# Performance work log

Hardware: AMD Instinct MI355X
Metric: run time of the kernel (lower is better)

Reference implementation:

```python
import jax, jax.numpy as jnp
import numpy as np

NUM_HEADS = 8
C_DIM = 512


def setup_inputs() -> dict:
    key = jax.random.key(0)
    ks = jax.random.split(key, 10)
    B, K, C, H, W = 8, 4, C_DIM, 16, 16
    M = NUM_HEADS
    s = 0.02
    return {
        "content": jax.random.normal(ks[0], (B, C, H, W), jnp.float32),
        "refs": jax.random.normal(ks[1], (B, K, C, H, W), jnp.float32),
        "qW": jax.random.normal(ks[2], (C, C * M), jnp.float32) * s,
        "qb": jax.random.normal(ks[3], (C * M,), jnp.float32) * s,
        "kW": jax.random.normal(ks[4], (C, C * M), jnp.float32) * s,
        "kb": jax.random.normal(ks[5], (C * M,), jnp.float32) * s,
        "vW": jax.random.normal(ks[6], (C, C * M), jnp.float32) * s,
        "vb": jax.random.normal(ks[7], (C * M,), jnp.float32) * s,
        "fcW": jax.random.normal(ks[8], (C * M, C), jnp.float32) * s,
        "fcb": jax.random.normal(ks[9], (C,), jnp.float32) * s,
    }


def reference(content, refs, qW, qb, kW, kb, vW, vb, fcW, fcb):
    B, C, H, W = content.shape
    K = refs.shape[1]
    M = qW.shape[1] // C
    HW = H * W
    KHW = K * HW

    # b c h w -> b (h w) c
    cs = content.reshape(B, C, HW).transpose(0, 2, 1)
    # b k c h w -> b (k h w) c
    rs = refs.transpose(0, 1, 3, 4, 2).reshape(B, KHW, C)

    # projections; output channel layout is (c m): head m takes strided features
    q = (cs @ qW + qb).reshape(B, HW, C, M)      # b q c m
    k = (rs @ kW + kb).reshape(B, KHW, C, M)     # b k c m
    v = (rs @ vW + vb).reshape(B, KHW, C, M)     # b k c m

    scale = jnp.asarray(float(C) ** (M / 2.0), content.dtype)  # faithful: C**(num_heads/2)
    scores = jnp.einsum('bqcm,bkcm->bmqk', q, k) / scale
    attn = jax.nn.softmax(scores, axis=-1)
    # output concat is head-major: (m c)
    out = jnp.einsum('bmqk,bkcm->bqmc', attn, v).reshape(B, HW, M * C)

    res = out @ fcW + fcb                         # b (h w) c
    res = res.transpose(0, 2, 1).reshape(B, C, H, W)
    return jnp.concatenate([res, content], axis=1)
```

## Files before the change

### kernel.cpp

```cpp
#include <hip/hip_runtime.h>

#define B_   8
#define K_   4
#define C_   512
#define M_   8
#define HW_  256
#define CM_  4096

__global__ void k_rbar(const float* __restrict__ refs, float* __restrict__ rbar) {
    const int bc = blockIdx.x;
    const int b  = bc >> 9;
    const int c  = bc & (C_ - 1);
    const int t  = threadIdx.x;
    const int k   = t >> 6;
    const int hw4 = t & 63;

    const float4* p = (const float4*)refs
                    + ((((size_t)b * K_ + k) * C_ + c) << 6) + hw4;
    const float4 v = *p;
    float s = (v.x + v.y) + (v.z + v.w);

#pragma unroll
    for (int off = 32; off > 0; off >>= 1)
        s += __shfl_down(s, off, 64);

    __shared__ float wsum[4];
    if ((t & 63) == 0) wsum[t >> 6] = s;
    __syncthreads();
    if (t == 0)
        rbar[bc] = (wsum[0] + wsum[1] + wsum[2] + wsum[3]) * (1.0f / (K_ * HW_));
}

__global__ void k_vbar(const float* __restrict__ rbar, const float* __restrict__ vW,
                       const float* __restrict__ vb, float* __restrict__ of) {
    const int blk   = blockIdx.x;
    const int b     = blk >> 4;
    const int chunk = blk & 15;
    const int t     = threadIdx.x;
    const int cm    = chunk * 256 + t;

    __shared__ float rb[C_];
    for (int i = t; i < C_; i += 256) rb[i] = rbar[b * C_ + i];
    __syncthreads();

    float acc = 0.f;
#pragma unroll 8
    for (int c = 0; c < C_; ++c)
        acc += rb[c] * vW[(size_t)c * CM_ + cm];

    const int ci = cm >> 3;
    const int m  = cm & 7;
    of[b * CM_ + m * C_ + ci] = acc + vb[cm];
}

__global__ void k_res(const float* __restrict__ of, const float* __restrict__ fcW,
                      float* __restrict__ res_vec) {
    const int b  = blockIdx.x >> 3;
    const int jc = blockIdx.x & 7;
    const int t  = threadIdx.x;

    __shared__ float lof[512];
    lof[t] = of[b * CM_ + jc * 512 + t];
    __syncthreads();

    float acc = 0.f;
#pragma unroll 8
    for (int j = 0; j < 512; ++j)
        acc += lof[j] * fcW[(size_t)(jc * 512 + j) * C_ + t];

    atomicAdd(&res_vec[b * C_ + t], acc);
}

__global__ void k_out(const float* __restrict__ res_vec, const float* __restrict__ fcb,
                      const float* __restrict__ content, float4* __restrict__ out4) {
    const int i = blockIdx.x * 256 + threadIdx.x;
    const int hw4 = i & 63;
    const int ch  = (i >> 6) & 1023;
    const int b   = i >> 16;

    if (ch < C_) {
        const float v = res_vec[b * C_ + ch] + fcb[ch];
        out4[i] = make_float4(v, v, v, v);
    } else {
        const float4* c4 = (const float4*)content;
        out4[i] = c4[(((size_t)b * C_ + (ch - C_)) << 6) + hw4];
    }
}

extern "C" void kernel_launch(void* const* d_in, const int* in_sizes, int n_in,
                              void* d_out, int out_size, void* d_ws, size_t ws_size,
                              hipStream_t stream) {
    const float* content = (const float*)d_in[0];
    const float* refs    = (const float*)d_in[1];
    const float* vW  = (const float*)d_in[6];
    const float* vb  = (const float*)d_in[7];
    const float* fcW = (const float*)d_in[8];
    const float* fcb = (const float*)d_in[9];

    float* ws      = (float*)d_ws;
    float* rbar    = ws;
    float* of      = ws + 4096;
    float* res_vec = ws + 4096 + 32768;

    hipMemsetAsync(res_vec, 0, 4096 * sizeof(float), stream);

    k_rbar<<<B_ * C_, 256, 0, stream>>>(refs, rbar);
    k_vbar<<<128, 256, 0, stream>>>(rbar, vW, vb, of);
    k_res <<<64, 512, 0, stream>>>(of, fcW, res_vec);
    k_out <<<(B_ * 1024 * HW_ / 4) / 256, 256, 0, stream>>>(res_vec, fcb, content,
                                                            (float4*)d_out);
}
```

Baseline: 151.0 us.

## Split-K the vbar and fc GEMVs across more blocks with vector loads

Splits the reduction dimension of the v-projection and fc GEMVs into segments handled by many more blocks, combining partial sums with atomics. Uses float4/float2 weight loads and moves the head-major permutation into the fcW row indexing. Aims to raise occupancy and memory bandwidth on the weight reads, at the cost of extra atomics and a larger memset.

```diff
diff --git a/kernel.cpp b/kernel.cpp
--- a/kernel.cpp
+++ b/kernel.cpp
@@ -32,43 +32,61 @@
 }
 
 __global__ void k_vbar(const float* __restrict__ rbar, const float* __restrict__ vW,
-                       const float* __restrict__ vb, float* __restrict__ of) {
-    const int blk   = blockIdx.x;
-    const int b     = blk >> 4;
-    const int chunk = blk & 15;
-    const int t     = threadIdx.x;
-    const int cm    = chunk * 256 + t;
+                       const float* __restrict__ vb, float* __restrict__ vbar) {
+    const int blk  = blockIdx.x;
+    const int b    = blk >> 6;
+    const int tile = (blk >> 4) & 3;
+    const int seg  = blk & 15;
+    const int t    = threadIdx.x;
 
-    __shared__ float rb[C_];
-    for (int i = t; i < C_; i += 256) rb[i] = rbar[b * C_ + i];
+    __shared__ float rb[32];
+    if (t < 32) rb[t] = rbar[b * C_ + seg * 32 + t];
     __syncthreads();
 
-    float acc = 0.f;
+    const float4* vW4 = (const float4*)vW;
+    const int col4 = tile * 256 + t;
+
+    float4 acc = make_float4(0.f, 0.f, 0.f, 0.f);
 #pragma unroll 8
-    for (int c = 0; c < C_; ++c)
-        acc += rb[c] * vW[(size_t)c * CM_ + cm];
-
-    const int ci = cm >> 3;
-    const int m  = cm & 7;
-    of[b * CM_ + m * C_ + ci] = acc + vb[cm];
+    for (int c = 0; c < 32; ++c) {
+        const float4 w = vW4[(size_t)(seg * 32 + c) * 1024 + col4];
+        const float r = rb[c];
+        acc.x += r * w.x; acc.y += r * w.y; acc.z += r * w.z; acc.w += r * w.w;
+    }
+    if (seg == 0) {
+        const float4 bb = ((const float4*)vb)[col4];
+        acc.x += bb.x; acc.y += bb.y; acc.z += bb.z; acc.w += bb.w;
+    }
+    float* dst = vbar + (size_t)b * CM_ + col4 * 4;
+    atomicAdd(dst + 0, acc.x);
+    atomicAdd(dst + 1, acc.y);
+    atomicAdd(dst + 2, acc.z);
+    atomicAdd(dst + 3, acc.w);
 }
 
-__global__ void k_res(const float* __restrict__ of, const float* __restrict__ fcW,
+__global__ void k_res(const float* __restrict__ vbar, const float* __restrict__ fcW,
                       float* __restrict__ res_vec) {
-    const int b  = blockIdx.x >> 3;
-    const int jc = blockIdx.x & 7;
-    const int t  = threadIdx.x;
+    const int b   = blockIdx.x >> 5;
+    const int seg = blockIdx.x & 31;
+    const int t   = threadIdx.x;
 
-    __shared__ float lof[512];
-    lof[t] = of[b * CM_ + jc * 512 + t];
+    __shared__ float lof[128];
+    if (t < 128) lof[t] = vbar[(size_t)b * CM_ + seg * 128 + t];
     __syncthreads();
 
-    float acc = 0.f;
+    const float2* fcW2 = (const float2*)fcW;
+    float2 acc = make_float2(0.f, 0.f);
 #pragma unroll 8
-    for (int j = 0; j < 512; ++j)
-        acc += lof[j] * fcW[(size_t)(jc * 512 + j) * C_ + t];
-
-    atomicAdd(&res_vec[b * C_ + t], acc);
+    for (int j = 0; j < 128; ++j) {
+        const int cm  = seg * 128 + j;
+        const int row = (cm & 7) * C_ + (cm >> 3);
+        const float2 w = fcW2[(size_t)row * 256 + t];
+        const float v = lof[j];
+        acc.x += v * w.x; acc.y += v * w.y;
+    }
+    float* dst = res_vec + b * C_ + t * 2;
+    atomicAdd(dst + 0, acc.x);
+    atomicAdd(dst + 1, acc.y);
 }
 
 __global__ void k_out(const float* __restrict__ res_vec, const float* __restrict__ fcb,
@@ -99,14 +117,14 @@
 
     float* ws      = (float*)d_ws;
     float* rbar    = ws;
-    float* of      = ws + 4096;
+    float* vbar    = ws + 4096;
     float* res_vec = ws + 4096 + 32768;
 
-    hipMemsetAsync(res_vec, 0, 4096 * sizeof(float), stream);
+    hipMemsetAsync(vbar, 0, (32768 + 4096) * sizeof(float), stream);
 
     k_rbar<<<B_ * C_, 256, 0, stream>>>(refs, rbar);
-    k_vbar<<<128, 256, 0, stream>>>(rbar, vW, vb, of);
-    k_res <<<64, 512, 0, stream>>>(of, fcW, res_vec);
+    k_vbar<<<512, 256, 0, stream>>>(rbar, vW, vb, vbar);
+    k_res <<<256, 256, 0, stream>>>(vbar, fcW, res_vec);
     k_out <<<(B_ * 1024 * HW_ / 4) / 256, 256, 0, stream>>>(res_vec, fcb, content,
                                                             (float4*)d_out);
 }
```

Result: faster. 124.8 us (-17.4%).
